# Performance work log

Hardware: AMD Instinct MI355X
Metric: run time of the kernel (lower is better)

Reference implementation:

```python
import jax, jax.numpy as jnp
import numpy as np

N = 512      # num nodes (target + context)
F = 256      # num_features
H = 256      # num_hids
NH = 8       # num_heads
L = 6        # num_layers
W = 2        # window_size
EEN = 16     # edge_encode_num
EDN = 128    # edge_dist_encode_num
LN_EPS = 1e-5


def setup_inputs() -> dict:
    key = jax.random.key(0)
    ks = iter(jax.random.split(key, 64))
    def nrm(shape, scale=0.02):
        return jax.random.normal(next(ks), shape, jnp.float32) * scale
    inp = {}
    inp["x"] = jax.random.normal(next(ks), (N, F), jnp.float32)
    inp["node_encodes"] = jax.random.randint(next(ks), (N, 2), 0, 16)
    inp["edge_encodes"] = jax.random.randint(next(ks), (N, N, W), 0, EEN * W)
    inp["edge_dist_encodes"] = jax.random.randint(next(ks), (N, N, 1), 0, EDN)
    inp["target_node_size"] = 128
    inp["context_nodes_size"] = N - 128
    inp["device"] = 0
    # parameters (linear weights stored [in, out]; x @ W + b)
    inp["W_feat"] = nrm((F, H)); inp["b_feat"] = jnp.zeros((H,), jnp.float32)
    inp["edge_emb"] = jax.random.normal(next(ks), (EEN * W, H), jnp.float32)
    inp["edge_dist_emb"] = jax.random.normal(next(ks), (EDN, H), jnp.float32)
    inp["W_ee"] = nrm((H, NH)); inp["b_ee"] = jnp.zeros((NH,), jnp.float32)
    inp["W_ed"] = nrm((H, NH)); inp["b_ed"] = jnp.zeros((NH,), jnp.float32)
    # per-layer stacked params
    inp["ln1_s"] = jnp.ones((L, H), jnp.float32); inp["ln1_b"] = jnp.zeros((L, H), jnp.float32)
    inp["Wq"] = nrm((L, H, H)); inp["bq"] = jnp.zeros((L, H), jnp.float32)
    inp["Wk"] = nrm((L, H, H)); inp["bk"] = jnp.zeros((L, H), jnp.float32)
    inp["Wv"] = nrm((L, H, H)); inp["bv"] = jnp.zeros((L, H), jnp.float32)
    inp["Wo"] = nrm((L, H, H)); inp["bo"] = jnp.zeros((L, H), jnp.float32)
    inp["ln2_s"] = jnp.ones((L, H), jnp.float32); inp["ln2_b"] = jnp.zeros((L, H), jnp.float32)
    inp["W1"] = nrm((L, H, H)); inp["b1"] = jnp.zeros((L, H), jnp.float32)  # ffn_size == hidden_size
    inp["W2"] = nrm((L, H, H)); inp["b2"] = jnp.zeros((L, H), jnp.float32)
    return inp


def _layernorm(x, s, b):
    m = x.mean(-1, keepdims=True)
    v = ((x - m) ** 2).mean(-1, keepdims=True)
    return (x - m) * jax.lax.rsqrt(v + LN_EPS) * s + b


def _emb_maxnorm(table, idx):
    # nn.Embedding(max_norm=True): looked-up rows renormed to L2 norm <= 1
    e = table[idx]
    n = jnp.linalg.norm(e, axis=-1, keepdims=True)
    return e * jnp.where(n > 1.0, 1.0 / (n + 1e-7), 1.0)


def _forward(x, edge_encodes, edge_dist_encodes,
             W_feat, b_feat, edge_emb, edge_dist_emb, W_ee, b_ee, W_ed, b_ed,
             ln1_s, ln1_b, Wq, bq, Wk, bk, Wv, bv, Wo, bo,
             ln2_s, ln2_b, W1, b1, W2, b2):
    h = (x @ W_feat + b_feat)[None]                       # [1, N, H]
    # Graphormer-style additive attention bias
    bias1 = _emb_maxnorm(edge_emb, edge_encodes).mean(axis=-2)       # [N, N, H]
    bias1 = bias1 @ W_ee + b_ee                                      # [N, N, NH]
    bias2 = _emb_maxnorm(edge_dist_emb, edge_dist_encodes[:, :, 0]) @ W_ed + b_ed
    attn_bias = (bias1 + bias2).transpose(2, 0, 1)[None]             # [1, NH, N, N]

    dk = H // NH
    scale = dk ** -0.5
    for l in range(L):
        y = _layernorm(h, ln1_s[l], ln1_b[l])
        q = (y @ Wq[l] + bq[l]).reshape(1, N, NH, dk).transpose(0, 2, 1, 3) * scale
        k = (y @ Wk[l] + bk[l]).reshape(1, N, NH, dk).transpose(0, 2, 1, 3)
        v = (y @ Wv[l] + bv[l]).reshape(1, N, NH, dk).transpose(0, 2, 1, 3)
        scores = jnp.einsum('bhqd,bhkd->bhqk', q, k) + attn_bias
        a = jax.nn.softmax(scores, axis=-1)
        o = jnp.einsum('bhqk,bhkd->bhqd', a, v).transpose(0, 2, 1, 3).reshape(1, N, H)
        h = h + (o @ Wo[l] + bo[l])
        y = _layernorm(h, ln2_s[l], ln2_b[l])
        y = jax.nn.gelu(y @ W1[l] + b1[l], approximate=False) @ W2[l] + b2[l]
        h = h + y
    return h[0]                                            # [N, H]


def reference(x, node_encodes, edge_encodes, edge_dist_encodes,
              target_node_size, context_nodes_size, device,
              W_feat, b_feat, edge_emb, edge_dist_emb, W_ee, b_ee, W_ed, b_ed,
              ln1_s, ln1_b, Wq, bq, Wk, bk, Wv, bv, Wo, bo,
              ln2_s, ln2_b, W1, b1, W2, b2):
    # node_encodes, target_node_size, context_nodes_size, device unused (as in original forward)
    return _forward(x, edge_encodes, edge_dist_encodes,
                    W_feat, b_feat, edge_emb, edge_dist_emb, W_ee, b_ee, W_ed, b_ed,
                    ln1_s, ln1_b, Wq, bq, Wk, bk, Wv, bv, Wo, bo,
                    ln2_s, ln2_b, W1, b1, W2, b2)
```

## Files before the change

### kernel.cpp

```cpp
#include <hip/hip_runtime.h>
#include <math.h>

#define NN 512
#define HD 256
#define NLAYER 6
#define QSCALE 0.17677669529663687f
#define ASTR 264

typedef __attribute__((ext_vector_type(8))) short bf16x8;
typedef __attribute__((ext_vector_type(4))) short bf16x4;
typedef __attribute__((ext_vector_type(4))) float f32x4;

__device__ __forceinline__ short f2bf(float f) {
  union { float f; unsigned u; } v; v.f = f;
  unsigned r = (v.u + 0x7FFFu + ((v.u >> 16) & 1u)) >> 16;
  return (short)r;
}
__device__ __forceinline__ float bf2f(short s) {
  union { unsigned u; float f; } v; v.u = ((unsigned)(unsigned short)s) << 16;
  return v.f;
}

__global__ __launch_bounds__(256) void prep1_kernel(
    const float* __restrict__ Wq, const float* __restrict__ Wk,
    const float* __restrict__ Wv, const float* __restrict__ Wo,
    const float* __restrict__ W1, const float* __restrict__ W2,
    const float* __restrict__ Wf,
    const float* __restrict__ edge_emb, const float* __restrict__ edge_dist_emb,
    const float* __restrict__ W_ee, const float* __restrict__ W_ed,
    short* __restrict__ Aqkv, short* __restrict__ AoT,
    short* __restrict__ A1T, short* __restrict__ A2T, short* __restrict__ WfT,
    float* __restrict__ eeP, float* __restrict__ edP) {
  int b = blockIdx.x, tid = threadIdx.x;
  if (b < 2368) {
    __shared__ float tile[32][33];
    const float* src; short* dst; float scl = 1.f;
    int t;
    if (b < 2304) {
      int l = b / 384; int rr = b % 384; int mat = rr / 64; t = rr % 64;
      if      (mat == 0) { src = Wq + l * 65536; dst = Aqkv + l * 196608; scl = QSCALE; }
      else if (mat == 1) { src = Wk + l * 65536; dst = Aqkv + l * 196608 + 65536; }
      else if (mat == 2) { src = Wv + l * 65536; dst = Aqkv + l * 196608 + 131072; }
      else if (mat == 3) { src = Wo + l * 65536; dst = AoT + l * 65536; }
      else if (mat == 4) { src = W1 + l * 65536; dst = A1T + l * 65536; }
      else               { src = W2 + l * 65536; dst = A2T + l * 65536; }
    } else {
      src = Wf; dst = WfT; t = b - 2304;
    }
    int tr = t >> 3, tc = t & 7;
    int kl = tid >> 3, nl4 = (tid & 7) * 4;
    float4 v = *(const float4*)(src + (tr * 32 + kl) * 256 + tc * 32 + nl4);
    tile[kl][nl4 + 0] = v.x; tile[kl][nl4 + 1] = v.y;
    tile[kl][nl4 + 2] = v.z; tile[kl][nl4 + 3] = v.w;
    __syncthreads();
    int nl = tid >> 3, kl4 = (tid & 7) * 4;
    bf16x4 o;
    #pragma unroll
    for (int i = 0; i < 4; i++) o[i] = f2bf(tile[kl4 + i][nl] * scl);
    *(bf16x4*)(dst + (tc * 32 + nl) * 256 + tr * 32 + kl4) = o;
  } else {
    int r = b - 2368;
    const float* table; const float* W; float* out; int row;
    if (r < 32) { table = edge_emb;      W = W_ee; out = eeP; row = r; }
    else        { table = edge_dist_emb; W = W_ed; out = edP; row = r - 32; }
    int w = tid >> 6, l = tid & 63;
    __shared__ float sb[4];
    float val = table[row * HD + tid];
    float ss = val * val;
    #pragma unroll
    for (int o = 32; o; o >>= 1) ss += __shfl_xor(ss, o);
    if (l == 0) sb[w] = ss;
    __syncthreads();
    ss = sb[0] + sb[1] + sb[2] + sb[3];
    float n = sqrtf(ss);
    float sc = (n > 1.f) ? 1.f / (n + 1e-7f) : 1.f;
    float v = val * sc;
    __syncthreads();
    #pragma unroll
    for (int hh = 0; hh < 8; hh++) {
      float p = v * W[tid * 8 + hh];
      #pragma unroll
      for (int o = 32; o; o >>= 1) p += __shfl_xor(p, o);
      if (l == 0) sb[w] = p;
      __syncthreads();
      if (tid == 0) out[row * 8 + hh] = sb[0] + sb[1] + sb[2] + sb[3];
      __syncthreads();
    }
  }
}

__global__ __launch_bounds__(512) void prep2_kernel(
    const int* __restrict__ ee, const int* __restrict__ ed,
    const float* __restrict__ eeP, const float* __restrict__ edP,
    const float* __restrict__ b_ee, const float* __restrict__ b_ed,
    short* __restrict__ bias_bf,
    const float* __restrict__ x, const short* __restrict__ WfT,
    const float* __restrict__ b_feat, float* __restrict__ h,
    const float* __restrict__ ln1_s, const float* __restrict__ ln1_b,
    const short* __restrict__ Aqkv, const float* __restrict__ bq,
    const float* __restrict__ bk, const float* __restrict__ bv,
    short* __restrict__ q_bf, short* __restrict__ k_bf, short* __restrict__ vT_bf) {
  __shared__ __align__(16) char lds_raw[17000];
  int tid = threadIdx.x, bid = blockIdx.x;
  if (bid < 512) {
    float* seeP = (float*)lds_raw;
    float* sedP = seeP + 256;
    float* sbe  = sedP + 1024;
    float* sbd  = sbe + 8;
    if (tid < 256) seeP[tid] = eeP[tid];
    sedP[tid] = edP[tid]; sedP[tid + 512] = edP[tid + 512];
    if (tid < 8) { sbe[tid] = b_ee[tid]; sbd[tid] = b_ed[tid]; }
    __syncthreads();
    int idx = bid * 512 + tid;
    int e0 = ee[idx * 2], e1 = ee[idx * 2 + 1];
    int d = ed[idx];
    #pragma unroll
    for (int hh = 0; hh < 8; hh++) {
      bias_bf[hh * (NN * NN) + idx] = f2bf(
          0.5f * (seeP[e0 * 8 + hh] + seeP[e1 * 8 + hh]) + sbe[hh]
          + sedP[d * 8 + hh] + sbd[hh]);
    }
    return;
  }
  short* Abuf = (short*)lds_raw;
  float* hbuf = (float*)(lds_raw + 8448);
  int w = tid >> 6, l = tid & 63, lr = l & 15, lk = l >> 4;
  int m0 = (bid - 512) * 8;
  if (tid < 264) {
    bf16x8 z = {};
    *(bf16x8*)(Abuf + 8 * ASTR + tid * 8) = z;
  }
  {
    int row = tid >> 6, j = tid & 63;
    float4 v = *(const float4*)(x + (m0 + row) * 256 + j * 4);
    bf16x4 o4; o4[0] = f2bf(v.x); o4[1] = f2bf(v.y); o4[2] = f2bf(v.z); o4[3] = f2bf(v.w);
    *(bf16x4*)(Abuf + row * ASTR + j * 4) = o4;
  }
  __syncthreads();
  {
    f32x4 acc[2] = {};
    int nb = w * 32;
    #pragma unroll
    for (int k0 = 0; k0 < 256; k0 += 32) {
      bf16x8 af = *(const bf16x8*)(Abuf + lr * ASTR + k0 + lk * 8);
      bf16x8 b0 = *(const bf16x8*)(WfT + (nb + lr) * 256 + k0 + lk * 8);
      bf16x8 b1f = *(const bf16x8*)(WfT + (nb + 16 + lr) * 256 + k0 + lk * 8);
      acc[0] = __builtin_amdgcn_mfma_f32_16x16x32_bf16(af, b0, acc[0], 0, 0, 0);
      acc[1] = __builtin_amdgcn_mfma_f32_16x16x32_bf16(af, b1f, acc[1], 0, 0, 0);
    }
    #pragma unroll
    for (int t = 0; t < 2; t++) {
      int n = nb + t * 16 + lr;
      #pragma unroll
      for (int r = 0; r < 4; r++) {
        int m = lk * 4 + r;
        if (m < 8) {
          float v = acc[t][r] + b_feat[n];
          hbuf[m * 256 + n] = v;
          h[(m0 + m) * 256 + n] = v;
        }
      }
    }
  }
  __syncthreads();
  {
    float4 v4 = *(const float4*)(hbuf + w * 256 + l * 4);
    float sum = v4.x + v4.y + v4.z + v4.w;
    #pragma unroll
    for (int o = 32; o; o >>= 1) sum += __shfl_xor(sum, o);
    float mean = sum * (1.f / 256.f);
    float dx = v4.x - mean, dy = v4.y - mean, dz = v4.z - mean, dw = v4.w - mean;
    float var = dx * dx + dy * dy + dz * dz + dw * dw;
    #pragma unroll
    for (int o = 32; o; o >>= 1) var += __shfl_xor(var, o);
    float inv = rsqrtf(var * (1.f / 256.f) + 1e-5f);
    const float4 sv = *(const float4*)(ln1_s + l * 4);
    const float4 bv4 = *(const float4*)(ln1_b + l * 4);
    bf16x4 o4;
    o4[0] = f2bf(dx * inv * sv.x + bv4.x);
    o4[1] = f2bf(dy * inv * sv.y + bv4.y);
    o4[2] = f2bf(dz * inv * sv.z + bv4.z);
    o4[3] = f2bf(dw * inv * sv.w + bv4.w);
    *(bf16x4*)(Abuf + w * ASTR + l * 4) = o4;
  }
  __syncthreads();
  {
    f32x4 acc[6] = {};
    int nb = w * 96;
    #pragma unroll 2
    for (int k0 = 0; k0 < 256; k0 += 32) {
      bf16x8 af = *(const bf16x8*)(Abuf + lr * ASTR + k0 + lk * 8);
      #pragma unroll
      for (int t = 0; t < 6; t++) {
        bf16x8 bfr = *(const bf16x8*)(Aqkv + (nb + t * 16 + lr) * 256 + k0 + lk * 8);
        acc[t] = __builtin_amdgcn_mfma_f32_16x16x32_bf16(af, bfr, acc[t], 0, 0, 0);
      }
    }
    #pragma unroll
    for (int t = 0; t < 6; t++) {
      int n = nb + t * 16 + lr;
      #pragma unroll
      for (int r = 0; r < 4; r++) {
        int m = lk * 4 + r;
        if (m < 8) {
          int gm = m0 + m;
          float v = acc[t][r];
          if (n < 256) {
            q_bf[((n >> 5) * 512 + gm) * 32 + (n & 31)] = f2bf(v + bq[n] * QSCALE);
          } else if (n < 512) {
            int nn = n - 256;
            k_bf[((nn >> 5) * 512 + gm) * 32 + (nn & 31)] = f2bf(v + bk[nn]);
          } else {
            int nn = n - 512;
            vT_bf[nn * 512 + gm] = f2bf(v + bv[nn]);
          }
        }
      }
    }
  }
}

__global__ __launch_bounds__(512) void attn_kernel(
    const short* __restrict__ q_bf, const short* __restrict__ k_bf,
    const short* __restrict__ vT_bf, const short* __restrict__ bias_bf,
    short* __restrict__ o_bf) {
  __shared__ __align__(16) short S[8 * 520];
  int tid = threadIdx.x, bid = blockIdx.x;
  int w = tid >> 6, l = tid & 63, lr = l & 15, lk = l >> 4;
  int head = bid >> 6, rt = bid & 63;
  {
    int row = tid >> 6, grp = tid & 63;
    *(bf16x8*)(S + row * 520 + grp * 8) =
        *(const bf16x8*)(bias_bf + (head * 512 + rt * 8 + row) * 512 + grp * 8);
  }
  bf16x8 aq = *(const bf16x8*)(q_bf + (head * 512 + rt * 8 + (lr & 7)) * 32 + lk * 8);
  __syncthreads();
  {
    f32x4 sacc[4];
    #pragma unroll
    for (int j = 0; j < 4; j++) {
      int node0 = w * 64 + j * 16;
      bf16x8 bk8 = *(const bf16x8*)(k_bf + (head * 512 + node0 + lr) * 32 + lk * 8);
      f32x4 s = {};
      sacc[j] = __builtin_amdgcn_mfma_f32_16x16x32_bf16(aq, bk8, s, 0, 0, 0);
    }
    #pragma unroll
    for (int j = 0; j < 4; j++) {
      int gnode = w * 64 + j * 16 + lr;
      #pragma unroll
      for (int r = 0; r < 4; r++) {
        int row = lk * 4 + r;
        if (row < 8) {
          short* sp = S + row * 520 + gnode;
          *sp = f2bf(sacc[j][r] + bf2f(*sp));
        }
      }
    }
  }
  __syncthreads();
  {
    short* Srow = S + w * 520;
    bf16x8 pk = *(const bf16x8*)(Srow + l * 8);
    float v[8];
    #pragma unroll
    for (int e = 0; e < 8; e++) v[e] = bf2f(pk[e]);
    float mx = -1e30f;
    #pragma unroll
    for (int i = 0; i < 8; i++) mx = fmaxf(mx, v[i]);
    #pragma unroll
    for (int o = 32; o; o >>= 1) mx = fmaxf(mx, __shfl_xor(mx, o));
    float sum = 0.f;
    #pragma unroll
    for (int i = 0; i < 8; i++) { v[i] = __expf(v[i] - mx); sum += v[i]; }
    #pragma unroll
    for (int o = 32; o; o >>= 1) sum += __shfl_xor(sum, o);
    float inv = 1.f / sum;
    bf16x8 po;
    #pragma unroll
    for (int e = 0; e < 8; e++) po[e] = f2bf(v[e] * inv);
    *(bf16x8*)(Srow + l * 8) = po;
  }
  __syncthreads();
  if (w < 2) {
    int dh = w;
    f32x4 oc0 = {}, oc1 = {};
    #pragma unroll
    for (int ch = 0; ch < 16; ch += 2) {
      bf16x8 ap0 = *(const bf16x8*)(S + (lr & 7) * 520 + ch * 32 + lk * 8);
      bf16x8 bv0 = *(const bf16x8*)(vT_bf + (head * 32 + dh * 16 + lr) * 512 + ch * 32 + lk * 8);
      bf16x8 ap1 = *(const bf16x8*)(S + (lr & 7) * 520 + (ch + 1) * 32 + lk * 8);
      bf16x8 bv1 = *(const bf16x8*)(vT_bf + (head * 32 + dh * 16 + lr) * 512 + (ch + 1) * 32 + lk * 8);
      oc0 = __builtin_amdgcn_mfma_f32_16x16x32_bf16(ap0, bv0, oc0, 0, 0, 0);
      oc1 = __builtin_amdgcn_mfma_f32_16x16x32_bf16(ap1, bv1, oc1, 0, 0, 0);
    }
    f32x4 oc = oc0 + oc1;
    #pragma unroll
    for (int r = 0; r < 4; r++) {
      int row = lk * 4 + r;
      if (row < 8)
        o_bf[(rt * 8 + row) * 256 + head * 32 + dh * 16 + lr] = f2bf(oc[r]);
    }
  }
}

__global__ __launch_bounds__(1024) void tail_kernel(
    const short* __restrict__ o_bf, float* __restrict__ h,
    const short* __restrict__ AoT_l, const float* __restrict__ bo_l,
    const float* __restrict__ ln2_s, const float* __restrict__ ln2_b,
    const short* __restrict__ A1T_l, const float* __restrict__ b1_l,
    const short* __restrict__ A2T_l, const float* __restrict__ b2_l,
    const float* __restrict__ ln1n_s, const float* __restrict__ ln1n_b,
    const short* __restrict__ Aqkv_n, const float* __restrict__ bq_n,
    const float* __restrict__ bk_n, const float* __restrict__ bv_n,
    short* __restrict__ q_bf, short* __restrict__ k_bf, short* __restrict__ vT_bf,
    int last) {
  __shared__ __align__(16) short Abuf[16 * ASTR];
  __shared__ __align__(16) short Bbuf[16 * ASTR];
  __shared__ __align__(16) float hbuf[2 * 256];
  int tid = threadIdx.x, bid = blockIdx.x;
  int w = tid >> 6, l = tid & 63, lr = l & 15, lk = l >> 4;
  int m0 = bid * 2;
  for (int i = tid; i < 924; i += 1024) {
    bf16x8 z = {};
    if (i < 462) *(bf16x8*)(Abuf + 2 * ASTR + i * 8) = z;
    else         *(bf16x8*)(Bbuf + 2 * ASTR + (i - 462) * 8) = z;
  }
  if (tid < 64) {
    int row = tid >> 5, j = tid & 31;
    *(bf16x8*)(Abuf + row * ASTR + j * 8) =
        *(const bf16x8*)(o_bf + (m0 + row) * 256 + j * 8);
  }
  __syncthreads();
  {
    f32x4 acc = {};
    int nb = w * 16;
    #pragma unroll
    for (int k0 = 0; k0 < 256; k0 += 32) {
      bf16x8 af = *(const bf16x8*)(Abuf + lr * ASTR + k0 + lk * 8);
      bf16x8 b0 = *(const bf16x8*)(AoT_l + (nb + lr) * 256 + k0 + lk * 8);
      acc = __builtin_amdgcn_mfma_f32_16x16x32_bf16(af, b0, acc, 0, 0, 0);
    }
    int n = nb + lr;
    #pragma unroll
    for (int r = 0; r < 4; r++) {
      int m = lk * 4 + r;
      if (m < 2) {
        float hv = h[(m0 + m) * 256 + n] + acc[r] + bo_l[n];
        hbuf[m * 256 + n] = hv;
        h[(m0 + m) * 256 + n] = hv;
      }
    }
  }
  __syncthreads();
  if (w < 2) {
    float4 v4 = *(const float4*)(hbuf + w * 256 + l * 4);
    float sum = v4.x + v4.y + v4.z + v4.w;
    #pragma unroll
    for (int o = 32; o; o >>= 1) sum += __shfl_xor(sum, o);
    float mean = sum * (1.f / 256.f);
    float dx = v4.x - mean, dy = v4.y - mean, dz = v4.z - mean, dw = v4.w - mean;
    float var = dx * dx + dy * dy + dz * dz + dw * dw;
    #pragma unroll
    for (int o = 32; o; o >>= 1) var += __shfl_xor(var, o);
    float inv = rsqrtf(var * (1.f / 256.f) + 1e-5f);
    const float4 sv = *(const float4*)(ln2_s + l * 4);
    const float4 bv4 = *(const float4*)(ln2_b + l * 4);
    bf16x4 o4;
    o4[0] = f2bf(dx * inv * sv.x + bv4.x);
    o4[1] = f2bf(dy * inv * sv.y + bv4.y);
    o4[2] = f2bf(dz * inv * sv.z + bv4.z);
    o4[3] = f2bf(dw * inv * sv.w + bv4.w);
    *(bf16x4*)(Abuf + w * ASTR + l * 4) = o4;
  }
  __syncthreads();
  {
    f32x4 acc = {};
    int nb = w * 16;
    #pragma unroll
    for (int k0 = 0; k0 < 256; k0 += 32) {
      bf16x8 af = *(const bf16x8*)(Abuf + lr * ASTR + k0 + lk * 8);
      bf16x8 b0 = *(const bf16x8*)(A1T_l + (nb + lr) * 256 + k0 + lk * 8);
      acc = __builtin_amdgcn_mfma_f32_16x16x32_bf16(af, b0, acc, 0, 0, 0);
    }
    int n = nb + lr;
    #pragma unroll
    for (int r = 0; r < 4; r++) {
      int m = lk * 4 + r;
      if (m < 2) {
        float val = acc[r] + b1_l[n];
        Bbuf[m * ASTR + n] =
            f2bf(0.5f * val * (1.f + erff(val * 0.70710678118654752f)));
      }
    }
  }
  __syncthreads();
  {
    f32x4 acc = {};
    int nb = w * 16;
    #pragma unroll
    for (int k0 = 0; k0 < 256; k0 += 32) {
      bf16x8 af = *(const bf16x8*)(Bbuf + lr * ASTR + k0 + lk * 8);
      bf16x8 b0 = *(const bf16x8*)(A2T_l + (nb + lr) * 256 + k0 + lk * 8);
      acc = __builtin_amdgcn_mfma_f32_16x16x32_bf16(af, b0, acc, 0, 0, 0);
    }
    int n = nb + lr;
    #pragma unroll
    for (int r = 0; r < 4; r++) {
      int m = lk * 4 + r;
      if (m < 2) {
        float hv = hbuf[m * 256 + n] + acc[r] + b2_l[n];
        h[(m0 + m) * 256 + n] = hv;
        hbuf[m * 256 + n] = hv;
      }
    }
  }
  if (last) return;
  __syncthreads();
  if (w < 2) {
    float4 v4 = *(const float4*)(hbuf + w * 256 + l * 4);
    float sum = v4.x + v4.y + v4.z + v4.w;
    #pragma unroll
    for (int o = 32; o; o >>= 1) sum += __shfl_xor(sum, o);
    float mean = sum * (1.f / 256.f);
    float dx = v4.x - mean, dy = v4.y - mean, dz = v4.z - mean, dw = v4.w - mean;
    float var = dx * dx + dy * dy + dz * dz + dw * dw;
    #pragma unroll
    for (int o = 32; o; o >>= 1) var += __shfl_xor(var, o);
    float inv = rsqrtf(var * (1.f / 256.f) + 1e-5f);
    const float4 sv = *(const float4*)(ln1n_s + l * 4);
    const float4 bv4 = *(const float4*)(ln1n_b + l * 4);
    bf16x4 o4;
    o4[0] = f2bf(dx * inv * sv.x + bv4.x);
    o4[1] = f2bf(dy * inv * sv.y + bv4.y);
    o4[2] = f2bf(dz * inv * sv.z + bv4.z);
    o4[3] = f2bf(dw * inv * sv.w + bv4.w);
    *(bf16x4*)(Abuf + w * ASTR + l * 4) = o4;
  }
  __syncthreads();
  {
    f32x4 acc[3] = {};
    int nb = w * 48;
    #pragma unroll 2
    for (int k0 = 0; k0 < 256; k0 += 32) {
      bf16x8 af = *(const bf16x8*)(Abuf + lr * ASTR + k0 + lk * 8);
      #pragma unroll
      for (int t = 0; t < 3; t++) {
        bf16x8 bfr = *(const bf16x8*)(Aqkv_n + (nb + t * 16 + lr) * 256 + k0 + lk * 8);
        acc[t] = __builtin_amdgcn_mfma_f32_16x16x32_bf16(af, bfr, acc[t], 0, 0, 0);
      }
    }
    #pragma unroll
    for (int t = 0; t < 3; t++) {
      int n = nb + t * 16 + lr;
      #pragma unroll
      for (int r = 0; r < 4; r++) {
        int m = lk * 4 + r;
        if (m < 2) {
          int gm = m0 + m;
          float v = acc[t][r];
          if (n < 256) {
            q_bf[((n >> 5) * 512 + gm) * 32 + (n & 31)] = f2bf(v + bq_n[n] * QSCALE);
          } else if (n < 512) {
            int nn = n - 256;
            k_bf[((nn >> 5) * 512 + gm) * 32 + (nn & 31)] = f2bf(v + bk_n[nn]);
          } else {
            int nn = n - 512;
            vT_bf[nn * 512 + gm] = f2bf(v + bv_n[nn]);
          }
        }
      }
    }
  }
}

extern "C" void kernel_launch(void* const* d_in, const int* in_sizes, int n_in,
                              void* d_out, int out_size, void* d_ws, size_t ws_size,
                              hipStream_t stream) {
  const float* x             = (const float*)d_in[0];
  const int*   edge_encodes  = (const int*)d_in[2];
  const int*   edge_dist_enc = (const int*)d_in[3];
  const float* W_feat = (const float*)d_in[7];
  const float* b_feat = (const float*)d_in[8];
  const float* edge_emb      = (const float*)d_in[9];
  const float* edge_dist_emb = (const float*)d_in[10];
  const float* W_ee = (const float*)d_in[11];
  const float* b_ee = (const float*)d_in[12];
  const float* W_ed = (const float*)d_in[13];
  const float* b_ed = (const float*)d_in[14];
  const float* ln1_s = (const float*)d_in[15];
  const float* ln1_b = (const float*)d_in[16];
  const float* Wq = (const float*)d_in[17];
  const float* bq = (const float*)d_in[18];
  const float* Wk = (const float*)d_in[19];
  const float* bk = (const float*)d_in[20];
  const float* Wv = (const float*)d_in[21];
  const float* bv = (const float*)d_in[22];
  const float* Wo = (const float*)d_in[23];
  const float* bo = (const float*)d_in[24];
  const float* ln2_s = (const float*)d_in[25];
  const float* ln2_b = (const float*)d_in[26];
  const float* W1 = (const float*)d_in[27];
  const float* b1 = (const float*)d_in[28];
  const float* W2 = (const float*)d_in[29];
  const float* b2 = (const float*)d_in[30];

  float* h = (float*)d_out;
  char* base = (char*)d_ws;
  short* bias_bf = (short*)base;
  short* Aqkv = (short*)(base + 4194304);
  short* AoT  = (short*)(base + 6553600);
  short* A1T  = (short*)(base + 7340032);
  short* A2T  = (short*)(base + 8126464);
  short* WfT  = (short*)(base + 8912896);
  short* q_bf = (short*)(base + 9043968);
  short* k_bf = (short*)(base + 9306112);
  short* vT_bf= (short*)(base + 9568256);
  short* o_bf = (short*)(base + 9830400);
  float* eeP  = (float*)(base + 10092544);
  float* edP  = (float*)(base + 10093568);

  prep1_kernel<<<2528, 256, 0, stream>>>(
      Wq, Wk, Wv, Wo, W1, W2, W_feat,
      edge_emb, edge_dist_emb, W_ee, W_ed,
      Aqkv, AoT, A1T, A2T, WfT, eeP, edP);
  prep2_kernel<<<576, 512, 0, stream>>>(
      edge_encodes, edge_dist_enc, eeP, edP, b_ee, b_ed, bias_bf,
      x, WfT, b_feat, h, ln1_s, ln1_b, Aqkv, bq, bk, bv, q_bf, k_bf, vT_bf);

  for (int l = 0; l < NLAYER; l++) {
    attn_kernel<<<512, 512, 0, stream>>>(q_bf, k_bf, vT_bf, bias_bf, o_bf);
    int ln = (l < NLAYER - 1) ? l + 1 : l;
    tail_kernel<<<256, 1024, 0, stream>>>(
        o_bf, h,
        AoT + l * 65536, bo + l * HD,
        ln2_s + l * HD, ln2_b + l * HD,
        A1T + l * 65536, b1 + l * HD,
        A2T + l * 65536, b2 + l * HD,
        ln1_s + ln * HD, ln1_b + ln * HD,
        Aqkv + ln * 196608, bq + ln * HD, bk + ln * HD, bv + ln * HD,
        q_bf, k_bf, vT_bf, l == NLAYER - 1);
  }
}
```

Measured before the change: 234.8 us.

## Fuse attention into per-row-pair layer kernel with ping-pong QKV buffers

Merges the separate attention kernel into the tail kernel, so each 1024-thread block computes attention for its two query rows across all 8 heads before running the output projection and FFN. The fused layer writes next-layer Q/K/V, so Q/K/V are double-buffered in ping-pong workspace to avoid read/write races between blocks. This removes one launch per layer and the o_bf global round trip. In exchange, each block runs MFMA tiles with only 2 of 16 rows useful in QK and PV, wasting matrix throughput, and K/V reads are repeated by 256 blocks.

Result: slower. 268.7 us (+14.4%).

```diff
diff --git a/kernel.cpp b/kernel.cpp
--- a/kernel.cpp
+++ b/kernel.cpp
@@ -220,91 +220,10 @@
   }
 }
 
-__global__ __launch_bounds__(512) void attn_kernel(
-    const short* __restrict__ q_bf, const short* __restrict__ k_bf,
-    const short* __restrict__ vT_bf, const short* __restrict__ bias_bf,
-    short* __restrict__ o_bf) {
-  __shared__ __align__(16) short S[8 * 520];
-  int tid = threadIdx.x, bid = blockIdx.x;
-  int w = tid >> 6, l = tid & 63, lr = l & 15, lk = l >> 4;
-  int head = bid >> 6, rt = bid & 63;
-  {
-    int row = tid >> 6, grp = tid & 63;
-    *(bf16x8*)(S + row * 520 + grp * 8) =
-        *(const bf16x8*)(bias_bf + (head * 512 + rt * 8 + row) * 512 + grp * 8);
-  }
-  bf16x8 aq = *(const bf16x8*)(q_bf + (head * 512 + rt * 8 + (lr & 7)) * 32 + lk * 8);
-  __syncthreads();
-  {
-    f32x4 sacc[4];
-    #pragma unroll
-    for (int j = 0; j < 4; j++) {
-      int node0 = w * 64 + j * 16;
-      bf16x8 bk8 = *(const bf16x8*)(k_bf + (head * 512 + node0 + lr) * 32 + lk * 8);
-      f32x4 s = {};
-      sacc[j] = __builtin_amdgcn_mfma_f32_16x16x32_bf16(aq, bk8, s, 0, 0, 0);
-    }
-    #pragma unroll
-    for (int j = 0; j < 4; j++) {
-      int gnode = w * 64 + j * 16 + lr;
-      #pragma unroll
-      for (int r = 0; r < 4; r++) {
-        int row = lk * 4 + r;
-        if (row < 8) {
-          short* sp = S + row * 520 + gnode;
-          *sp = f2bf(sacc[j][r] + bf2f(*sp));
-        }
-      }
-    }
-  }
-  __syncthreads();
-  {
-    short* Srow = S + w * 520;
-    bf16x8 pk = *(const bf16x8*)(Srow + l * 8);
-    float v[8];
-    #pragma unroll
-    for (int e = 0; e < 8; e++) v[e] = bf2f(pk[e]);
-    float mx = -1e30f;
-    #pragma unroll
-    for (int i = 0; i < 8; i++) mx = fmaxf(mx, v[i]);
-    #pragma unroll
-    for (int o = 32; o; o >>= 1) mx = fmaxf(mx, __shfl_xor(mx, o));
-    float sum = 0.f;
-    #pragma unroll
-    for (int i = 0; i < 8; i++) { v[i] = __expf(v[i] - mx); sum += v[i]; }
-    #pragma unroll
-    for (int o = 32; o; o >>= 1) sum += __shfl_xor(sum, o);
-    float inv = 1.f / sum;
-    bf16x8 po;
-    #pragma unroll
-    for (int e = 0; e < 8; e++) po[e] = f2bf(v[e] * inv);
-    *(bf16x8*)(Srow + l * 8) = po;
-  }
-  __syncthreads();
-  if (w < 2) {
-    int dh = w;
-    f32x4 oc0 = {}, oc1 = {};
-    #pragma unroll
-    for (int ch = 0; ch < 16; ch += 2) {
-      bf16x8 ap0 = *(const bf16x8*)(S + (lr & 7) * 520 + ch * 32 + lk * 8);
-      bf16x8 bv0 = *(const bf16x8*)(vT_bf + (head * 32 + dh * 16 + lr) * 512 + ch * 32 + lk * 8);
-      bf16x8 ap1 = *(const bf16x8*)(S + (lr & 7) * 520 + (ch + 1) * 32 + lk * 8);
-      bf16x8 bv1 = *(const bf16x8*)(vT_bf + (head * 32 + dh * 16 + lr) * 512 + (ch + 1) * 32 + lk * 8);
-      oc0 = __builtin_amdgcn_mfma_f32_16x16x32_bf16(ap0, bv0, oc0, 0, 0, 0);
-      oc1 = __builtin_amdgcn_mfma_f32_16x16x32_bf16(ap1, bv1, oc1, 0, 0, 0);
-    }
-    f32x4 oc = oc0 + oc1;
-    #pragma unroll
-    for (int r = 0; r < 4; r++) {
-      int row = lk * 4 + r;
-      if (row < 8)
-        o_bf[(rt * 8 + row) * 256 + head * 32 + dh * 16 + lr] = f2bf(oc[r]);
-    }
-  }
-}
-
-__global__ __launch_bounds__(1024) void tail_kernel(
-    const short* __restrict__ o_bf, float* __restrict__ h,
+__global__ __launch_bounds__(1024) void layer_kernel(
+    const short* __restrict__ qin, const short* __restrict__ kin,
+    const short* __restrict__ vin, const short* __restrict__ bias_bf,
+    float* __restrict__ h,
     const short* __restrict__ AoT_l, const float* __restrict__ bo_l,
     const float* __restrict__ ln2_s, const float* __restrict__ ln2_b,
     const short* __restrict__ A1T_l, const float* __restrict__ b1_l,
@@ -312,25 +231,102 @@
     const float* __restrict__ ln1n_s, const float* __restrict__ ln1n_b,
     const short* __restrict__ Aqkv_n, const float* __restrict__ bq_n,
     const float* __restrict__ bk_n, const float* __restrict__ bv_n,
-    short* __restrict__ q_bf, short* __restrict__ k_bf, short* __restrict__ vT_bf,
+    short* __restrict__ qo, short* __restrict__ ko, short* __restrict__ vo,
     int last) {
+  __shared__ __align__(16) short S[16 * 520];
   __shared__ __align__(16) short Abuf[16 * ASTR];
   __shared__ __align__(16) short Bbuf[16 * ASTR];
   __shared__ __align__(16) float hbuf[2 * 256];
   int tid = threadIdx.x, bid = blockIdx.x;
   int w = tid >> 6, l = tid & 63, lr = l & 15, lk = l >> 4;
   int m0 = bid * 2;
+
   for (int i = tid; i < 924; i += 1024) {
     bf16x8 z = {};
     if (i < 462) *(bf16x8*)(Abuf + 2 * ASTR + i * 8) = z;
     else         *(bf16x8*)(Bbuf + 2 * ASTR + (i - 462) * 8) = z;
   }
-  if (tid < 64) {
-    int row = tid >> 5, j = tid & 31;
-    *(bf16x8*)(Abuf + row * ASTR + j * 8) =
-        *(const bf16x8*)(o_bf + (m0 + row) * 256 + j * 8);
-  }
-  __syncthreads();
+  {
+    int hr = tid >> 6, grp = tid & 63;
+    *(bf16x8*)(S + hr * 520 + grp * 8) =
+        *(const bf16x8*)(bias_bf + (hr >> 1) * 262144 + (m0 + (hr & 1)) * 512 + grp * 8);
+  }
+  __syncthreads();
+
+  {
+    int head = w >> 1, half = w & 1;
+    bf16x8 aq = *(const bf16x8*)(qin + (head * 512 + m0 + (lr & 1)) * 32 + lk * 8);
+    #pragma unroll
+    for (int pass = 0; pass < 2; pass++) {
+      f32x4 sacc[8];
+      #pragma unroll
+      for (int j = 0; j < 8; j++) {
+        int node0 = half * 256 + pass * 128 + j * 16;
+        bf16x8 bk8 = *(const bf16x8*)(kin + (head * 512 + node0 + lr) * 32 + lk * 8);
+        f32x4 s = {};
+        sacc[j] = __builtin_amdgcn_mfma_f32_16x16x32_bf16(aq, bk8, s, 0, 0, 0);
+      }
+      if (lk == 0) {
+        #pragma unroll
+        for (int j = 0; j < 8; j++) {
+          int gnode = half * 256 + pass * 128 + j * 16 + lr;
+          #pragma unroll
+          for (int r = 0; r < 2; r++) {
+            short* sp = S + (head * 2 + r) * 520 + gnode;
+            *sp = f2bf(sacc[j][r] + bf2f(*sp));
+          }
+        }
+      }
+    }
+  }
+  __syncthreads();
+
+  {
+    short* Srow = S + w * 520;
+    bf16x8 pk = *(const bf16x8*)(Srow + l * 8);
+    float v[8];
+    #pragma unroll
+    for (int e = 0; e < 8; e++) v[e] = bf2f(pk[e]);
+    float mx = -1e30f;
+    #pragma unroll
+    for (int i = 0; i < 8; i++) mx = fmaxf(mx, v[i]);
+    #pragma unroll
+    for (int o = 32; o; o >>= 1) mx = fmaxf(mx, __shfl_xor(mx, o));
+    float sum = 0.f;
+    #pragma unroll
+    for (int i = 0; i < 8; i++) { v[i] = __expf(v[i] - mx); sum += v[i]; }
+    #pragma unroll
+    for (int o = 32; o; o >>= 1) sum += __shfl_xor(sum, o);
+    float inv = 1.f / sum;
+    bf16x8 po;
+    #pragma unroll
+    for (int e = 0; e < 8; e++) po[e] = f2bf(v[e] * inv);
+    *(bf16x8*)(Srow + l * 8) = po;
+  }
+  __syncthreads();
+
+  {
+    int head = w >> 1, dh = w & 1;
+    f32x4 oc0 = {}, oc1 = {};
+    #pragma unroll
+    for (int ch = 0; ch < 16; ch += 2) {
+      bf16x8 ap0 = *(const bf16x8*)(S + (head * 2 + (lr & 1)) * 520 + ch * 32 + lk * 8);
+      bf16x8 bv0 = *(const bf16x8*)(vin + (head * 32 + dh * 16 + lr) * 512 + ch * 32 + lk * 8);
+      bf16x8 ap1 = *(const bf16x8*)(S + (head * 2 + (lr & 1)) * 520 + (ch + 1) * 32 + lk * 8);
+      bf16x8 bv1 = *(const bf16x8*)(vin + (head * 32 + dh * 16 + lr) * 512 + (ch + 1) * 32 + lk * 8);
+      oc0 = __builtin_amdgcn_mfma_f32_16x16x32_bf16(ap0, bv0, oc0, 0, 0, 0);
+      oc1 = __builtin_amdgcn_mfma_f32_16x16x32_bf16(ap1, bv1, oc1, 0, 0, 0);
+    }
+    f32x4 oc = oc0 + oc1;
+    #pragma unroll
+    for (int r = 0; r < 4; r++) {
+      int row = lk * 4 + r;
+      if (row < 2)
+        Abuf[row * ASTR + head * 32 + dh * 16 + lr] = f2bf(oc[r]);
+    }
+  }
+  __syncthreads();
+
   {
     f32x4 acc = {};
     int nb = w * 16;
@@ -459,13 +455,13 @@
           int gm = m0 + m;
           float v = acc[t][r];
           if (n < 256) {
-            q_bf[((n >> 5) * 512 + gm) * 32 + (n & 31)] = f2bf(v + bq_n[n] * QSCALE);
+            qo[((n >> 5) * 512 + gm) * 32 + (n & 31)] = f2bf(v + bq_n[n] * QSCALE);
           } else if (n < 512) {
             int nn = n - 256;
-            k_bf[((nn >> 5) * 512 + gm) * 32 + (nn & 31)] = f2bf(v + bk_n[nn]);
+            ko[((nn >> 5) * 512 + gm) * 32 + (nn & 31)] = f2bf(v + bk_n[nn]);
           } else {
             int nn = n - 512;
-            vT_bf[nn * 512 + gm] = f2bf(v + bv_n[nn]);
+            vo[nn * 512 + gm] = f2bf(v + bv_n[nn]);
           }
         }
       }
@@ -512,12 +508,13 @@
   short* A1T  = (short*)(base + 7340032);
   short* A2T  = (short*)(base + 8126464);
   short* WfT  = (short*)(base + 8912896);
-  short* q_bf = (short*)(base + 9043968);
-  short* k_bf = (short*)(base + 9306112);
-  short* vT_bf= (short*)(base + 9568256);
-  short* o_bf = (short*)(base + 9830400);
-  float* eeP  = (float*)(base + 10092544);
-  float* edP  = (float*)(base + 10093568);
+  short* qkv0 = (short*)(base + 9043968);
+  short* qkv1 = (short*)(base + 9830400);
+  float* eeP  = (float*)(base + 10616832);
+  float* edP  = (float*)(base + 10617856);
+
+  short* q0 = qkv0, *k0 = qkv0 + 131072, *v0 = qkv0 + 262144;
+  short* q1 = qkv1, *k1 = qkv1 + 131072, *v1 = qkv1 + 262144;
 
   prep1_kernel<<<2528, 256, 0, stream>>>(
       Wq, Wk, Wv, Wo, W1, W2, W_feat,
@@ -525,19 +522,21 @@
       Aqkv, AoT, A1T, A2T, WfT, eeP, edP);
   prep2_kernel<<<576, 512, 0, stream>>>(
       edge_encodes, edge_dist_enc, eeP, edP, b_ee, b_ed, bias_bf,
-      x, WfT, b_feat, h, ln1_s, ln1_b, Aqkv, bq, bk, bv, q_bf, k_bf, vT_bf);
+      x, WfT, b_feat, h, ln1_s, ln1_b, Aqkv, bq, bk, bv, q0, k0, v0);
 
   for (int l = 0; l < NLAYER; l++) {
-    attn_kernel<<<512, 512, 0, stream>>>(q_bf, k_bf, vT_bf, bias_bf, o_bf);
+    int p = l & 1;
+    short* qi = p ? q1 : q0; short* ki = p ? k1 : k0; short* vi = p ? v1 : v0;
+    short* qq = p ? q0 : q1; short* kk = p ? k0 : k1; short* vv = p ? v0 : v1;
     int ln = (l < NLAYER - 1) ? l + 1 : l;
-    tail_kernel<<<256, 1024, 0, stream>>>(
-        o_bf, h,
+    layer_kernel<<<256, 1024, 0, stream>>>(
+        qi, ki, vi, bias_bf, h,
         AoT + l * 65536, bo + l * HD,
         ln2_s + l * HD, ln2_b + l * HD,
         A1T + l * 65536, b1 + l * HD,
         A2T + l * 65536, b2 + l * HD,
         ln1_s + ln * HD, ln1_b + ln * HD,
         Aqkv + ln * 196608, bq + ln * HD, bk + ln * HD, bv + ln * HD,
-        q_bf, k_bf, vT_bf, l == NLAYER - 1);
+        qq, kk, vv, l == NLAYER - 1);
   }
 }
```
